# Performance work log

Hardware: AMD Instinct MI355X
Metric: run time of the kernel (lower is better)

The kernel has to match this reference:

```python
import jax, jax.numpy as jnp
import numpy as np

N_EMBD = 1024
HEAD_SIZE = 128


def setup_inputs() -> dict:
    key = jax.random.key(0)
    k_x, k_w, k_cov, k_b = jax.random.split(key, 4)
    x = jax.random.normal(k_x, (16384, 2, N_EMBD), dtype=jnp.float32)
    # values_proj: nn.Linear(n_embd, head_size, bias=False) -> weight [head_size, n_embd]
    W = jax.random.normal(k_w, (HEAD_SIZE, N_EMBD), dtype=jnp.float32) * (N_EMBD ** -0.5)
    cov = jax.random.normal(k_cov, (HEAD_SIZE, HEAD_SIZE), dtype=jnp.float32) * (HEAD_SIZE ** -0.5)
    bias = jax.random.normal(k_b, (HEAD_SIZE,), dtype=jnp.float32)
    return {"x": x, "W": W, "cov": cov, "bias": bias}


def reference(x, W, cov, bias):
    # x: [B, 2, E]; W: [H, E]; cov: [H, H]; bias: [H]
    values = jnp.einsum('be,he->bh', x[:, 0, :], W)  # [B, H]
    mask = jnp.einsum('be,he->bh', x[:, 1, :], W)    # [B, H]
    # diag_embed(mask) @ cov == mask[:, :, None] * cov  -> [B, H, H]
    coeffs = jax.nn.softmax(mask[:, :, None] * cov[None, :, :], axis=-1)
    # values.unsqueeze(1) @ coeffs + bias, then [:, 0, :]
    out = jnp.einsum('bh,bhk->bk', values, coeffs) + bias
    return out
```

## Files before the change

kernel.cpp:

```cpp
#include <hip/hip_runtime.h>

#define LOG2E 1.4426950408889634f

typedef __attribute__((ext_vector_type(8))) short frag_ab;
typedef __attribute__((ext_vector_type(4))) float frag_cd;

__device__ inline short f2bf(float f) {
    union { float f; unsigned u; } v; v.f = f;
    unsigned r = v.u + 0x7fffu + ((v.u >> 16) & 1u);
    return (short)(r >> 16);
}

template<int CTRL>
__device__ inline float dpp_ror_add(float x) {
    int t = __builtin_amdgcn_update_dpp(0, __builtin_bit_cast(int, x), CTRL, 0xf, 0xf, false);
    return x + __builtin_bit_cast(float, t);
}

#define GLD_TO_LDS(gp, lp)                                                              \
    __builtin_amdgcn_global_load_lds((const __attribute__((address_space(1))) void*)(gp), \
                                     (__attribute__((address_space(3))) void*)(lp), 16, 0, 0)

__global__ __launch_bounds__(256) void prep_kernel(const float* __restrict__ W,
                                                   short* __restrict__ wbf) {
    int g = blockIdx.x * 256 + threadIdx.x;
    int h = g >> 7;
    int k0 = (g & 127) << 3;
    const float* src = W + h * 1024 + k0;
    float4 w0 = *(const float4*)src;
    float4 w1 = *(const float4*)(src + 4);
    frag_ab af;
    af[0] = f2bf(w0.x); af[1] = f2bf(w0.y); af[2] = f2bf(w0.z); af[3] = f2bf(w0.w);
    af[4] = f2bf(w1.x); af[5] = f2bf(w1.y); af[6] = f2bf(w1.z); af[7] = f2bf(w1.w);
    int c = k0 >> 6, s = (k0 >> 5) & 1, kg = (k0 >> 3) & 3;
    int nt = h >> 4, m = h & 15, lane = kg * 16 + m;
    int dst = (((c * 8 + nt) * 2 + s) * 64 + lane) * 8;
    *(frag_ab*)(wbf + dst) = af;
}

__global__ __launch_bounds__(256, 4) void fused_kernel(const float* __restrict__ x,
                                                       const short* __restrict__ wbf,
                                                       const float* __restrict__ cov,
                                                       const float* __restrict__ bias,
                                                       float* __restrict__ out) {
    __shared__ __align__(16) char smem[32768];

    const int tid = threadIdx.x;
    const int lane = tid & 63, wave = tid >> 6;
    const int m = lane & 15, kg = lane >> 4;
    const long rowbase = (long)blockIdx.x * 64 + wave * 16;
    const float* xrow = x + (rowbase + m) * 1024 + kg * 8;

    const float bias_own = bias[tid & 127];

    frag_cd acc[8];
#pragma unroll
    for (int nt = 0; nt < 8; ++nt) acc[nt] = (frag_cd){0.f, 0.f, 0.f, 0.f};

    {
        const char* wc = (const char*)wbf;
        char* bd = smem;
        GLD_TO_LDS(wc + tid * 16,         bd + tid * 16);
        GLD_TO_LDS(wc + 4096 + tid * 16,  bd + 4096 + tid * 16);
        GLD_TO_LDS(wc + 8192 + tid * 16,  bd + 8192 + tid * 16);
        GLD_TO_LDS(wc + 12288 + tid * 16, bd + 12288 + tid * 16);
    }
    float4 a0 = *(const float4*)(xrow);
    float4 a1 = *(const float4*)(xrow + 4);
    float4 a2 = *(const float4*)(xrow + 32);
    float4 a3 = *(const float4*)(xrow + 36);
    __syncthreads();

    int cb = 0;
    for (int c = 0; c < 16; ++c) {
        float4 n0, n1, n2, n3;
        if (c < 15) {
            const char* wc = (const char*)wbf + (c + 1) * 16384;
            char* bd = smem + (cb ^ 1) * 16384;
            GLD_TO_LDS(wc + tid * 16,         bd + tid * 16);
            GLD_TO_LDS(wc + 4096 + tid * 16,  bd + 4096 + tid * 16);
            GLD_TO_LDS(wc + 8192 + tid * 16,  bd + 8192 + tid * 16);
            GLD_TO_LDS(wc + 12288 + tid * 16, bd + 12288 + tid * 16);
            const float* xn = xrow + (c + 1) * 64;
            n0 = *(const float4*)(xn);
            n1 = *(const float4*)(xn + 4);
            n2 = *(const float4*)(xn + 32);
            n3 = *(const float4*)(xn + 36);
        }
        frag_ab af0, af1;
        af0[0] = f2bf(a0.x); af0[1] = f2bf(a0.y); af0[2] = f2bf(a0.z); af0[3] = f2bf(a0.w);
        af0[4] = f2bf(a1.x); af0[5] = f2bf(a1.y); af0[6] = f2bf(a1.z); af0[7] = f2bf(a1.w);
        af1[0] = f2bf(a2.x); af1[1] = f2bf(a2.y); af1[2] = f2bf(a2.z); af1[3] = f2bf(a2.w);
        af1[4] = f2bf(a3.x); af1[5] = f2bf(a3.y); af1[6] = f2bf(a3.z); af1[7] = f2bf(a3.w);

        const char* bs = smem + cb * 16384;
#pragma unroll
        for (int nt = 0; nt < 8; ++nt) {
            frag_ab bf0 = *(const frag_ab*)(bs + (nt * 2 + 0) * 1024 + lane * 16);
            acc[nt] = __builtin_amdgcn_mfma_f32_16x16x32_bf16(af0, bf0, acc[nt], 0, 0, 0);
            frag_ab bf1 = *(const frag_ab*)(bs + (nt * 2 + 1) * 1024 + lane * 16);
            acc[nt] = __builtin_amdgcn_mfma_f32_16x16x32_bf16(af1, bf1, acc[nt], 0, 0, 0);
        }
        if (c < 15) { a0 = n0; a1 = n1; a2 = n2; a3 = n3; }
        __syncthreads();
        cb ^= 1;
    }

    const int i = tid >> 4;
    const int j = tid & 15;
    float covreg[8][8];
#pragma unroll
    for (int hh = 0; hh < 8; ++hh) {
        const float* cr = cov + (long)(i * 8 + hh) * 128 + j * 8;
        float4 c0 = *(const float4*)cr;
        float4 c1 = *(const float4*)(cr + 4);
        covreg[hh][0] = LOG2E * c0.x; covreg[hh][1] = LOG2E * c0.y;
        covreg[hh][2] = LOG2E * c0.z; covreg[hh][3] = LOG2E * c0.w;
        covreg[hh][4] = LOG2E * c1.x; covreg[hh][5] = LOG2E * c1.y;
        covreg[hh][6] = LOG2E * c1.z; covreg[hh][7] = LOG2E * c1.w;
    }
#pragma unroll
    for (int hh = 0; hh < 8; ++hh)
        asm volatile("" : "+v"(covreg[hh][0]), "+v"(covreg[hh][1]), "+v"(covreg[hh][2]),
                          "+v"(covreg[hh][3]), "+v"(covreg[hh][4]), "+v"(covreg[hh][5]),
                          "+v"(covreg[hh][6]), "+v"(covreg[hh][7]));

    float* vmf  = (float*)smem;
    float* obuf = vmf + 16 * 132;
    const long outbase = (long)blockIdx.x * 32 * 128;

    for (int w = 0; w < 4; ++w) {
        if (wave == w) {
#pragma unroll
            for (int nt = 0; nt < 8; ++nt)
#pragma unroll
                for (int r = 0; r < 4; ++r)
                    vmf[(kg * 4 + r) * 132 + nt * 16 + m] = acc[nt][r];
        }
        __syncthreads();

        for (int r2 = 0; r2 < 4; ++r2) {
#pragma unroll
            for (int sb = 0; sb < 2; ++sb) {
                const int lb = r2 * 2 + sb;
                const float* vrow = vmf + (2 * lb) * 132 + i * 8;
                const float* mrow = vmf + (2 * lb + 1) * 132 + i * 8;
                float4 v0  = *(const float4*)(vrow);
                float4 v1  = *(const float4*)(vrow + 4);
                float4 mk0 = *(const float4*)(mrow);
                float4 mk1 = *(const float4*)(mrow + 4);
                float vh[8] = {v0.x, v0.y, v0.z, v0.w, v1.x, v1.y, v1.z, v1.w};
                float mh[8] = {mk0.x, mk0.y, mk0.z, mk0.w, mk1.x, mk1.y, mk1.z, mk1.w};
                float op[8] = {0.f, 0.f, 0.f, 0.f, 0.f, 0.f, 0.f, 0.f};
#pragma unroll
                for (int hh = 0; hh < 8; ++hh) {
                    float mv = mh[hh];
                    float p[8];
#pragma unroll
                    for (int kk = 0; kk < 8; ++kk)
                        p[kk] = __builtin_amdgcn_exp2f(mv * covreg[hh][kk]);
                    float s0 = p[0] + p[1], s1 = p[2] + p[3];
                    float s2 = p[4] + p[5], s3 = p[6] + p[7];
                    float lsum = (s0 + s1) + (s2 + s3);
                    lsum = dpp_ror_add<0x121>(lsum);
                    lsum = dpp_ror_add<0x122>(lsum);
                    lsum = dpp_ror_add<0x124>(lsum);
                    lsum = dpp_ror_add<0x128>(lsum);
                    float wgt = vh[hh] * __builtin_amdgcn_rcpf(lsum);
#pragma unroll
                    for (int kk = 0; kk < 8; ++kk) op[kk] = fmaf(wgt, p[kk], op[kk]);
                }
                *(float4*)(obuf + (sb * 16 + i) * 132 + j * 8)     = make_float4(op[0], op[1], op[2], op[3]);
                *(float4*)(obuf + (sb * 16 + i) * 132 + j * 8 + 4) = make_float4(op[4], op[5], op[6], op[7]);
            }
            __syncthreads();
            {
                const int k  = tid & 127;
                const int s0 = tid >> 7;
                float o = bias_own;
#pragma unroll
                for (int ii = 0; ii < 16; ++ii) o += obuf[(s0 * 16 + ii) * 132 + k];
                out[outbase + (w * 8 + r2 * 2 + s0) * 128 + k] = o;
            }
            __syncthreads();
        }
    }
}

extern "C" void kernel_launch(void* const* d_in, const int* in_sizes, int n_in,
                              void* d_out, int out_size, void* d_ws, size_t ws_size,
                              hipStream_t stream) {
    const float* x    = (const float*)d_in[0];
    const float* W    = (const float*)d_in[1];
    const float* cov  = (const float*)d_in[2];
    const float* bias = (const float*)d_in[3];
    float* out = (float*)d_out;

    const int B = in_sizes[0] / (2 * 1024);

    short* wbf = (short*)d_ws;

    prep_kernel<<<64, 256, 0, stream>>>(W, wbf);
    fused_kernel<<<(2 * B) / 64, 256, 0, stream>>>(x, wbf, cov, bias, out);
}
```

Baseline: 276.8 us.

## Split fused kernel into projection and softmax-combine kernels with deeper x prefetch

Splits the single fused kernel into a GEMM projection kernel that writes values/mask to a global workspace and a separate combine kernel that does the softmax-weighted reduction. The projection loop is unrolled by two chunks, so x loads are prefetched two chunks ahead, and occupancy is relaxed to 2 blocks per SM. This aims to stop the serialized per-wave epilogue from stalling the memory-bound GEMM and to give the exp-heavy combine its own grid. The cost is an extra global round-trip of the [2B,128] intermediate and an additional launch.

```diff
diff --git a/kernel.cpp b/kernel.cpp
--- a/kernel.cpp
+++ b/kernel.cpp
@@ -20,6 +20,10 @@
 #define GLD_TO_LDS(gp, lp)                                                              \
     __builtin_amdgcn_global_load_lds((const __attribute__((address_space(1))) void*)(gp), \
                                      (__attribute__((address_space(3))) void*)(lp), 16, 0, 0)
+
+#define PACK_AF(af, p0, p1)                                                   \
+    af[0] = f2bf(p0.x); af[1] = f2bf(p0.y); af[2] = f2bf(p0.z); af[3] = f2bf(p0.w); \
+    af[4] = f2bf(p1.x); af[5] = f2bf(p1.y); af[6] = f2bf(p1.z); af[7] = f2bf(p1.w);
 
 __global__ __launch_bounds__(256) void prep_kernel(const float* __restrict__ W,
                                                    short* __restrict__ wbf) {
@@ -30,19 +34,16 @@
     float4 w0 = *(const float4*)src;
     float4 w1 = *(const float4*)(src + 4);
     frag_ab af;
-    af[0] = f2bf(w0.x); af[1] = f2bf(w0.y); af[2] = f2bf(w0.z); af[3] = f2bf(w0.w);
-    af[4] = f2bf(w1.x); af[5] = f2bf(w1.y); af[6] = f2bf(w1.z); af[7] = f2bf(w1.w);
+    PACK_AF(af, w0, w1);
     int c = k0 >> 6, s = (k0 >> 5) & 1, kg = (k0 >> 3) & 3;
     int nt = h >> 4, m = h & 15, lane = kg * 16 + m;
     int dst = (((c * 8 + nt) * 2 + s) * 64 + lane) * 8;
     *(frag_ab*)(wbf + dst) = af;
 }
 
-__global__ __launch_bounds__(256, 4) void fused_kernel(const float* __restrict__ x,
-                                                       const short* __restrict__ wbf,
-                                                       const float* __restrict__ cov,
-                                                       const float* __restrict__ bias,
-                                                       float* __restrict__ out) {
+__global__ __launch_bounds__(256, 2) void proj_kernel(const float* __restrict__ x,
+                                                      const short* __restrict__ wbf,
+                                                      float* __restrict__ vm) {
     __shared__ __align__(16) char smem[32768];
 
     const int tid = threadIdx.x;
@@ -51,63 +52,112 @@
     const long rowbase = (long)blockIdx.x * 64 + wave * 16;
     const float* xrow = x + (rowbase + m) * 1024 + kg * 8;
 
-    const float bias_own = bias[tid & 127];
-
     frag_cd acc[8];
 #pragma unroll
     for (int nt = 0; nt < 8; ++nt) acc[nt] = (frag_cd){0.f, 0.f, 0.f, 0.f};
 
     {
         const char* wc = (const char*)wbf;
-        char* bd = smem;
-        GLD_TO_LDS(wc + tid * 16,         bd + tid * 16);
-        GLD_TO_LDS(wc + 4096 + tid * 16,  bd + 4096 + tid * 16);
-        GLD_TO_LDS(wc + 8192 + tid * 16,  bd + 8192 + tid * 16);
-        GLD_TO_LDS(wc + 12288 + tid * 16, bd + 12288 + tid * 16);
-    }
-    float4 a0 = *(const float4*)(xrow);
-    float4 a1 = *(const float4*)(xrow + 4);
-    float4 a2 = *(const float4*)(xrow + 32);
-    float4 a3 = *(const float4*)(xrow + 36);
+        GLD_TO_LDS(wc + tid * 16,         smem + tid * 16);
+        GLD_TO_LDS(wc + 4096 + tid * 16,  smem + 4096 + tid * 16);
+        GLD_TO_LDS(wc + 8192 + tid * 16,  smem + 8192 + tid * 16);
+        GLD_TO_LDS(wc + 12288 + tid * 16, smem + 12288 + tid * 16);
+    }
+    float4 aA0 = *(const float4*)(xrow);
+    float4 aA1 = *(const float4*)(xrow + 4);
+    float4 aA2 = *(const float4*)(xrow + 32);
+    float4 aA3 = *(const float4*)(xrow + 36);
+    float4 aB0 = *(const float4*)(xrow + 64);
+    float4 aB1 = *(const float4*)(xrow + 68);
+    float4 aB2 = *(const float4*)(xrow + 96);
+    float4 aB3 = *(const float4*)(xrow + 100);
     __syncthreads();
 
     int cb = 0;
-    for (int c = 0; c < 16; ++c) {
-        float4 n0, n1, n2, n3;
-        if (c < 15) {
-            const char* wc = (const char*)wbf + (c + 1) * 16384;
+#pragma unroll
+    for (int cc = 0; cc < 8; ++cc) {
+        const int c0 = 2 * cc, c1 = 2 * cc + 1;
+        {
+            const char* wc = (const char*)wbf + (c0 + 1) * 16384;
             char* bd = smem + (cb ^ 1) * 16384;
             GLD_TO_LDS(wc + tid * 16,         bd + tid * 16);
             GLD_TO_LDS(wc + 4096 + tid * 16,  bd + 4096 + tid * 16);
             GLD_TO_LDS(wc + 8192 + tid * 16,  bd + 8192 + tid * 16);
             GLD_TO_LDS(wc + 12288 + tid * 16, bd + 12288 + tid * 16);
-            const float* xn = xrow + (c + 1) * 64;
-            n0 = *(const float4*)(xn);
-            n1 = *(const float4*)(xn + 4);
-            n2 = *(const float4*)(xn + 32);
-            n3 = *(const float4*)(xn + 36);
-        }
-        frag_ab af0, af1;
-        af0[0] = f2bf(a0.x); af0[1] = f2bf(a0.y); af0[2] = f2bf(a0.z); af0[3] = f2bf(a0.w);
-        af0[4] = f2bf(a1.x); af0[5] = f2bf(a1.y); af0[6] = f2bf(a1.z); af0[7] = f2bf(a1.w);
-        af1[0] = f2bf(a2.x); af1[1] = f2bf(a2.y); af1[2] = f2bf(a2.z); af1[3] = f2bf(a2.w);
-        af1[4] = f2bf(a3.x); af1[5] = f2bf(a3.y); af1[6] = f2bf(a3.z); af1[7] = f2bf(a3.w);
-
-        const char* bs = smem + cb * 16384;
-#pragma unroll
-        for (int nt = 0; nt < 8; ++nt) {
-            frag_ab bf0 = *(const frag_ab*)(bs + (nt * 2 + 0) * 1024 + lane * 16);
-            acc[nt] = __builtin_amdgcn_mfma_f32_16x16x32_bf16(af0, bf0, acc[nt], 0, 0, 0);
-            frag_ab bf1 = *(const frag_ab*)(bs + (nt * 2 + 1) * 1024 + lane * 16);
-            acc[nt] = __builtin_amdgcn_mfma_f32_16x16x32_bf16(af1, bf1, acc[nt], 0, 0, 0);
-        }
-        if (c < 15) { a0 = n0; a1 = n1; a2 = n2; a3 = n3; }
-        __syncthreads();
-        cb ^= 1;
-    }
-
+
+            frag_ab af0, af1;
+            PACK_AF(af0, aA0, aA1);
+            PACK_AF(af1, aA2, aA3);
+            if (c0 + 2 < 16) {
+                const float* xn = xrow + (c0 + 2) * 64;
+                aA0 = *(const float4*)(xn);
+                aA1 = *(const float4*)(xn + 4);
+                aA2 = *(const float4*)(xn + 32);
+                aA3 = *(const float4*)(xn + 36);
+            }
+            const char* bs = smem + cb * 16384;
+#pragma unroll
+            for (int nt = 0; nt < 8; ++nt) {
+                frag_ab bf0 = *(const frag_ab*)(bs + (nt * 2 + 0) * 1024 + lane * 16);
+                acc[nt] = __builtin_amdgcn_mfma_f32_16x16x32_bf16(af0, bf0, acc[nt], 0, 0, 0);
+                frag_ab bf1 = *(const frag_ab*)(bs + (nt * 2 + 1) * 1024 + lane * 16);
+                acc[nt] = __builtin_amdgcn_mfma_f32_16x16x32_bf16(af1, bf1, acc[nt], 0, 0, 0);
+            }
+            __syncthreads();
+            cb ^= 1;
+        }
+        {
+            if (c1 < 15) {
+                const char* wc = (const char*)wbf + (c1 + 1) * 16384;
+                char* bd = smem + (cb ^ 1) * 16384;
+                GLD_TO_LDS(wc + tid * 16,         bd + tid * 16);
+                GLD_TO_LDS(wc + 4096 + tid * 16,  bd + 4096 + tid * 16);
+                GLD_TO_LDS(wc + 8192 + tid * 16,  bd + 8192 + tid * 16);
+                GLD_TO_LDS(wc + 12288 + tid * 16, bd + 12288 + tid * 16);
+            }
+            frag_ab af0, af1;
+            PACK_AF(af0, aB0, aB1);
+            PACK_AF(af1, aB2, aB3);
+            if (c1 + 2 < 16) {
+                const float* xn = xrow + (c1 + 2) * 64;
+                aB0 = *(const float4*)(xn);
+                aB1 = *(const float4*)(xn + 4);
+                aB2 = *(const float4*)(xn + 32);
+                aB3 = *(const float4*)(xn + 36);
+            }
+            const char* bs = smem + cb * 16384;
+#pragma unroll
+            for (int nt = 0; nt < 8; ++nt) {
+                frag_ab bf0 = *(const frag_ab*)(bs + (nt * 2 + 0) * 1024 + lane * 16);
+                acc[nt] = __builtin_amdgcn_mfma_f32_16x16x32_bf16(af0, bf0, acc[nt], 0, 0, 0);
+                frag_ab bf1 = *(const frag_ab*)(bs + (nt * 2 + 1) * 1024 + lane * 16);
+                acc[nt] = __builtin_amdgcn_mfma_f32_16x16x32_bf16(af1, bf1, acc[nt], 0, 0, 0);
+            }
+            __syncthreads();
+            cb ^= 1;
+        }
+    }
+
+#pragma unroll
+    for (int nt = 0; nt < 8; ++nt)
+#pragma unroll
+        for (int r = 0; r < 4; ++r) {
+            long row = rowbase + kg * 4 + r;
+            vm[row * 128 + nt * 16 + m] = acc[nt][r];
+        }
+}
+
+__global__ __launch_bounds__(256, 4) void combine_kernel(const float* __restrict__ vm,
+                                                         const float* __restrict__ cov,
+                                                         const float* __restrict__ bias,
+                                                         float* __restrict__ out) {
+    __shared__ float obuf[2][16][132];
+
+    const int tid = threadIdx.x;
     const int i = tid >> 4;
     const int j = tid & 15;
+    const float bias_own = bias[tid & 127];
+
     float covreg[8][8];
 #pragma unroll
     for (int hh = 0; hh < 8; ++hh) {
@@ -125,65 +175,51 @@
                           "+v"(covreg[hh][3]), "+v"(covreg[hh][4]), "+v"(covreg[hh][5]),
                           "+v"(covreg[hh][6]), "+v"(covreg[hh][7]));
 
-    float* vmf  = (float*)smem;
-    float* obuf = vmf + 16 * 132;
-    const long outbase = (long)blockIdx.x * 32 * 128;
-
-    for (int w = 0; w < 4; ++w) {
-        if (wave == w) {
-#pragma unroll
-            for (int nt = 0; nt < 8; ++nt)
-#pragma unroll
-                for (int r = 0; r < 4; ++r)
-                    vmf[(kg * 4 + r) * 132 + nt * 16 + m] = acc[nt][r];
+    const long b0 = (long)blockIdx.x * 8;
+    for (int rr = 0; rr < 4; ++rr) {
+#pragma unroll
+        for (int sb = 0; sb < 2; ++sb) {
+            const long b = b0 + rr * 2 + sb;
+            const float* vrow = vm + (2 * b) * 128 + i * 8;
+            const float* mrow = vm + (2 * b + 1) * 128 + i * 8;
+            float4 v0  = *(const float4*)(vrow);
+            float4 v1  = *(const float4*)(vrow + 4);
+            float4 mk0 = *(const float4*)(mrow);
+            float4 mk1 = *(const float4*)(mrow + 4);
+            float vh[8] = {v0.x, v0.y, v0.z, v0.w, v1.x, v1.y, v1.z, v1.w};
+            float mh[8] = {mk0.x, mk0.y, mk0.z, mk0.w, mk1.x, mk1.y, mk1.z, mk1.w};
+            float op[8] = {0.f, 0.f, 0.f, 0.f, 0.f, 0.f, 0.f, 0.f};
+#pragma unroll
+            for (int hh = 0; hh < 8; ++hh) {
+                float mv = mh[hh];
+                float p[8];
+#pragma unroll
+                for (int kk = 0; kk < 8; ++kk)
+                    p[kk] = __builtin_amdgcn_exp2f(mv * covreg[hh][kk]);
+                float s0 = p[0] + p[1], s1 = p[2] + p[3];
+                float s2 = p[4] + p[5], s3 = p[6] + p[7];
+                float lsum = (s0 + s1) + (s2 + s3);
+                lsum = dpp_ror_add<0x121>(lsum);
+                lsum = dpp_ror_add<0x122>(lsum);
+                lsum = dpp_ror_add<0x124>(lsum);
+                lsum = dpp_ror_add<0x128>(lsum);
+                float w = vh[hh] * __builtin_amdgcn_rcpf(lsum);
+#pragma unroll
+                for (int kk = 0; kk < 8; ++kk) op[kk] = fmaf(w, p[kk], op[kk]);
+            }
+            *(float4*)&obuf[sb][i][j * 8]     = make_float4(op[0], op[1], op[2], op[3]);
+            *(float4*)&obuf[sb][i][j * 8 + 4] = make_float4(op[4], op[5], op[6], op[7]);
         }
         __syncthreads();
-
-        for (int r2 = 0; r2 < 4; ++r2) {
-#pragma unroll
-            for (int sb = 0; sb < 2; ++sb) {
-                const int lb = r2 * 2 + sb;
-                const float* vrow = vmf + (2 * lb) * 132 + i * 8;
-                const float* mrow = vmf + (2 * lb + 1) * 132 + i * 8;
-                float4 v0  = *(const float4*)(vrow);
-                float4 v1  = *(const float4*)(vrow + 4);
-                float4 mk0 = *(const float4*)(mrow);
-                float4 mk1 = *(const float4*)(mrow + 4);
-                float vh[8] = {v0.x, v0.y, v0.z, v0.w, v1.x, v1.y, v1.z, v1.w};
-                float mh[8] = {mk0.x, mk0.y, mk0.z, mk0.w, mk1.x, mk1.y, mk1.z, mk1.w};
-                float op[8] = {0.f, 0.f, 0.f, 0.f, 0.f, 0.f, 0.f, 0.f};
-#pragma unroll
-                for (int hh = 0; hh < 8; ++hh) {
-                    float mv = mh[hh];
-                    float p[8];
-#pragma unroll
-                    for (int kk = 0; kk < 8; ++kk)
-                        p[kk] = __builtin_amdgcn_exp2f(mv * covreg[hh][kk]);
-                    float s0 = p[0] + p[1], s1 = p[2] + p[3];
-                    float s2 = p[4] + p[5], s3 = p[6] + p[7];
-                    float lsum = (s0 + s1) + (s2 + s3);
-                    lsum = dpp_ror_add<0x121>(lsum);
-                    lsum = dpp_ror_add<0x122>(lsum);
-                    lsum = dpp_ror_add<0x124>(lsum);
-                    lsum = dpp_ror_add<0x128>(lsum);
-                    float wgt = vh[hh] * __builtin_amdgcn_rcpf(lsum);
-#pragma unroll
-                    for (int kk = 0; kk < 8; ++kk) op[kk] = fmaf(wgt, p[kk], op[kk]);
-                }
-                *(float4*)(obuf + (sb * 16 + i) * 132 + j * 8)     = make_float4(op[0], op[1], op[2], op[3]);
-                *(float4*)(obuf + (sb * 16 + i) * 132 + j * 8 + 4) = make_float4(op[4], op[5], op[6], op[7]);
-            }
-            __syncthreads();
-            {
-                const int k  = tid & 127;
-                const int s0 = tid >> 7;
-                float o = bias_own;
-#pragma unroll
-                for (int ii = 0; ii < 16; ++ii) o += obuf[(s0 * 16 + ii) * 132 + k];
-                out[outbase + (w * 8 + r2 * 2 + s0) * 128 + k] = o;
-            }
-            __syncthreads();
-        }
+        {
+            const int k  = tid & 127;
+            const int s0 = tid >> 7;
+            float o = bias_own;
+#pragma unroll
+            for (int ii = 0; ii < 16; ++ii) o += obuf[s0][ii][k];
+            out[(b0 + rr * 2 + s0) * 128 + k] = o;
+        }
+        __syncthreads();
     }
 }
 
@@ -199,7 +235,9 @@
     const int B = in_sizes[0] / (2 * 1024);
 
     short* wbf = (short*)d_ws;
+    float* vm  = (float*)(wbf + 128 * 1024);
 
     prep_kernel<<<64, 256, 0, stream>>>(W, wbf);
-    fused_kernel<<<(2 * B) / 64, 256, 0, stream>>>(x, wbf, cov, bias, out);
-}
+    proj_kernel<<<(2 * B) / 64, 256, 0, stream>>>(x, wbf, vm);
+    combine_kernel<<<B / 8, 256, 0, stream>>>(vm, cov, bias, out);
+}
```

After: 261.6 us. 1.06x faster.
